# Kernel tuning notes

Measured on AMD Instinct MI355X. Metric: run time of the kernel, lower is better.

## Reference

```python
import jax, jax.numpy as jnp
import numpy as np

SCALE = 8.0  # sqrt(d_head=64)
NEG = -1e9


def setup_inputs() -> dict:
    key = jax.random.key(0)
    kq, kk, kv, km = jax.random.split(key, 4)
    B, H, S, D = 2, 16, 2048, 64
    q = jax.random.normal(kq, (B, H, S, D), dtype=jnp.float32)
    k = jax.random.normal(kk, (B, H, S, D), dtype=jnp.float32)
    v = jax.random.normal(kv, (B, H, S, D), dtype=jnp.float32)
    mask = jax.random.randint(km, (B, 1, 1, S), 0, 2, dtype=jnp.int32)
    return {"q": q, "k": k, "v": v, "mask": mask}


def reference(q, k, v, mask):
    # scores: [B,H,S,S]
    scores = jnp.einsum("bhqd,bhkd->bhqk", q / SCALE, k)
    scores = jnp.where(mask == 0, NEG, scores)
    attn = jax.nn.softmax(scores, axis=-1)  # dropout p=0 -> identity
    out = jnp.einsum("bhqk,bhkd->bhqd", attn, v)
    return (out, attn)
```

## Files before the change

### kernel.cpp

```cpp
#include <hip/hip_runtime.h>
#include <hip/hip_bf16.h>


#define S_LEN 2048
#define DH 64
#define QT 128
#define NCH (S_LEN / 64)

typedef __attribute__((ext_vector_type(8))) short  s16x8;
typedef __attribute__((ext_vector_type(8))) __bf16 bf16x8;
typedef __attribute__((ext_vector_type(4))) float  f32x4;
typedef __attribute__((ext_vector_type(2))) unsigned int u32x2;

__device__ __forceinline__ short f2bf(float x) {
    __hip_bfloat16 h = __float2bfloat16(x);
    return *reinterpret_cast<short*>(&h);
}
__device__ __forceinline__ unsigned pack2(float a, float b) {
    return (unsigned)(unsigned short)f2bf(a) | ((unsigned)(unsigned short)f2bf(b) << 16);
}
__device__ __forceinline__ bf16x8 ldfrag(const short* p) {
    s16x8 t = *(const s16x8*)p;
    return __builtin_bit_cast(bf16x8, t);
}
__device__ __forceinline__ int SW(int r, int c) { return r * 64 + (c ^ ((r & 7) << 3)); }

__global__ __launch_bounds__(512, 4) void sdpa_kernel(
    const float* __restrict__ q, const float* __restrict__ k,
    const float* __restrict__ v, const int* __restrict__ mask,
    float* __restrict__ out, float* __restrict__ attn)
{
    __shared__ __align__(16) short shQ[QT * 64];
    __shared__ __align__(16) short shK[2][64 * 64];
    __shared__ __align__(16) short shVt[2][64 * 64];
    __shared__ __align__(16) short shP[8][16 * 64];
    __shared__ __align__(16) float shMaskF[S_LEN];

    const int tid  = threadIdx.x;
    const int lane = tid & 63;
    const int w    = tid >> 6;
    const int l15  = lane & 15;
    const int lg   = lane >> 4;

    const int bh = blockIdx.y;
    const int b  = bh >> 4;
    const int q0 = blockIdx.x * QT;

    const float* qbase = q + ((size_t)bh * S_LEN + q0) * DH;
    const float* kbase = k + (size_t)bh * S_LEN * DH;
    const float* vbase = v + (size_t)bh * S_LEN * DH;
    float* attnbh = attn + (size_t)bh * S_LEN * S_LEN;

    for (int i = tid; i < S_LEN; i += 512)
        shMaskF[i] = (mask[b * S_LEN + i] != 0) ? 1.0f : 0.0f;
    {
        const int row = tid >> 2;
        const int d0  = (tid & 3) * 16;
        const float* src = qbase + row * DH + d0;
        const float4 a = *(const float4*)(src);
        const float4 bq = *(const float4*)(src + 4);
        const float4 c = *(const float4*)(src + 8);
        const float4 d = *(const float4*)(src + 12);
        s16x8 v0, v1;
        v0[0]=f2bf(a.x*0.125f);  v0[1]=f2bf(a.y*0.125f);  v0[2]=f2bf(a.z*0.125f);  v0[3]=f2bf(a.w*0.125f);
        v0[4]=f2bf(bq.x*0.125f); v0[5]=f2bf(bq.y*0.125f); v0[6]=f2bf(bq.z*0.125f); v0[7]=f2bf(bq.w*0.125f);
        v1[0]=f2bf(c.x*0.125f);  v1[1]=f2bf(c.y*0.125f);  v1[2]=f2bf(c.z*0.125f);  v1[3]=f2bf(c.w*0.125f);
        v1[4]=f2bf(d.x*0.125f);  v1[5]=f2bf(d.y*0.125f);  v1[6]=f2bf(d.z*0.125f);  v1[7]=f2bf(d.w*0.125f);
        *(s16x8*)&shQ[SW(row, d0)]     = v0;
        *(s16x8*)&shQ[SW(row, d0 + 8)] = v1;
    }

    const int krow = tid >> 3;
    const int kd0  = (tid & 7) * 8;
    auto loadK = [&](int c0, float4& a, float4& bb) {
        const float* src = kbase + (size_t)(c0 + krow) * DH + kd0;
        a  = *(const float4*)(src);
        bb = *(const float4*)(src + 4);
    };
    auto writeK = [&](short* dst, const float4& a, const float4& bb) {
        s16x8 vv;
        vv[0]=f2bf(a.x);  vv[1]=f2bf(a.y);  vv[2]=f2bf(a.z);  vv[3]=f2bf(a.w);
        vv[4]=f2bf(bb.x); vv[5]=f2bf(bb.y); vv[6]=f2bf(bb.z); vv[7]=f2bf(bb.w);
        *(s16x8*)&dst[SW(krow, kd0)] = vv;
    };
    const int vr0 = (tid & 31) * 2;
    const int vdg = tid >> 5;
    auto loadV = [&](int c0, float4& a, float4& bb) {
        const float* src = vbase + (size_t)(c0 + vr0) * DH + vdg * 4;
        a  = *(const float4*)(src);
        bb = *(const float4*)(src + DH);
    };
    auto writeVt = [&](short* dst, const float4& a, const float4& bb) {
        const float av[4] = {a.x, a.y, a.z, a.w};
        const float bv[4] = {bb.x, bb.y, bb.z, bb.w};
        int* dw = (int*)dst;
#pragma unroll
        for (int i = 0; i < 4; ++i) {
            const int d = vdg * 4 + i;
            dw[(d * 64 + (vr0 ^ ((d & 7) << 3))) >> 1] = (int)pack2(av[i], bv[i]);
        }
    };

    float4 ka, kb;
    loadK(0, ka, kb);
    writeK(shK[0], ka, kb);
    __syncthreads();

    const int qrow = w * 16 + l15;
    const bf16x8 qf0 = ldfrag(&shQ[SW(qrow, 8 * lg)]);
    const bf16x8 qf1 = ldfrag(&shQ[SW(qrow, 32 + 8 * lg)]);

    auto qkT = [&](const short* K, f32x4* s) {
#pragma unroll
        for (int ct = 0; ct < 4; ++ct) {
            const int kc = ct * 16 + l15;
            bf16x8 kf = ldfrag(&K[SW(kc, 8 * lg)]);
            s[ct] = __builtin_amdgcn_mfma_f32_16x16x32_bf16(kf, qf0, s[ct], 0, 0, 0);
            kf = ldfrag(&K[SW(kc, 32 + 8 * lg)]);
            s[ct] = __builtin_amdgcn_mfma_f32_16x16x32_bf16(kf, qf1, s[ct], 0, 0, 0);
        }
    };

    float lacc = 0.f;
    for (int t = 0; t < NCH; ++t) {
        const int cur = t & 1;
        if (t + 1 < NCH) loadK((t + 1) * 64, ka, kb);
        __syncthreads();
        f32x4 s[4] = {{0,0,0,0},{0,0,0,0},{0,0,0,0},{0,0,0,0}};
        qkT(shK[cur], s);
        const int c0 = t * 64;
#pragma unroll
        for (int ct = 0; ct < 4; ++ct) {
            const f32x4 mf = *(const f32x4*)&shMaskF[c0 + ct * 16 + lg * 4];
#pragma unroll
            for (int r = 0; r < 4; ++r)
                lacc = fmaf(__expf(s[ct][r]), mf[r], lacc);
        }
        if (t + 1 < NCH) writeK(shK[cur ^ 1], ka, kb);
    }
    lacc += __shfl_xor(lacc, 16);
    lacc += __shfl_xor(lacc, 32);
    const float lnInvl = -__logf(lacc);

    f32x4 oacc[4] = {{0,0,0,0},{0,0,0,0},{0,0,0,0},{0,0,0,0}};
    float4 va, vb;
    loadK(0, ka, kb);
    loadV(0, va, vb);
    writeK(shK[0], ka, kb);
    writeVt(shVt[0], va, vb);

    short* const shPw = shP[w];
    for (int t = 0; t < NCH; ++t) {
        const int cur = t & 1;
        if (t + 1 < NCH) { loadK((t + 1) * 64, ka, kb); loadV((t + 1) * 64, va, vb); }
        __syncthreads();
        f32x4 s[4] = {{0,0,0,0},{0,0,0,0},{0,0,0,0},{0,0,0,0}};
        qkT(shK[cur], s);

        const int c0 = t * 64;
        float* abase = attnbh + (size_t)(q0 + qrow) * S_LEN + c0;
#pragma unroll
        for (int ct = 0; ct < 4; ++ct) {
            const f32x4 mf = *(const f32x4*)&shMaskF[c0 + ct * 16 + lg * 4];
            f32x4 p;
#pragma unroll
            for (int r = 0; r < 4; ++r)
                p[r] = __expf(s[ct][r] + lnInvl) * mf[r];
            __builtin_nontemporal_store(p, (f32x4*)(abase + ct * 16 + lg * 4));
            u32x2 pk;
            pk[0] = pack2(p[0], p[1]);
            pk[1] = pack2(p[2], p[3]);
            *(u32x2*)&shPw[SW(l15, ct * 16 + lg * 4)] = pk;
        }
#pragma unroll
        for (int g = 0; g < 2; ++g) {
            const bf16x8 pf = ldfrag(&shPw[SW(l15, g * 32 + 8 * lg)]);
#pragma unroll
            for (int dt = 0; dt < 4; ++dt) {
                const bf16x8 af = ldfrag(&shVt[cur][SW(dt * 16 + l15, g * 32 + 8 * lg)]);
                oacc[dt] = __builtin_amdgcn_mfma_f32_16x16x32_bf16(af, pf, oacc[dt], 0, 0, 0);
            }
        }
        if (t + 1 < NCH) { writeK(shK[cur ^ 1], ka, kb); writeVt(shVt[cur ^ 1], va, vb); }
    }

    float* obase = out + ((size_t)bh * S_LEN + q0 + qrow) * DH;
#pragma unroll
    for (int dt = 0; dt < 4; ++dt)
        __builtin_nontemporal_store(oacc[dt], (f32x4*)(obase + dt * 16 + lg * 4));
}

extern "C" void kernel_launch(void* const* d_in, const int* in_sizes, int n_in,
                              void* d_out, int out_size, void* d_ws, size_t ws_size,
                              hipStream_t stream)
{
    const float* q    = (const float*)d_in[0];
    const float* k    = (const float*)d_in[1];
    const float* v    = (const float*)d_in[2];
    const int*   mask = (const int*)d_in[3];
    float* out  = (float*)d_out;
    float* attn = out + (size_t)2 * 16 * 2048 * 64;

    dim3 grid(S_LEN / QT, 2 * 16);
    sdpa_kernel<<<grid, dim3(512), 0, stream>>>(q, k, v, mask, out, attn);
}
```

Measured before the change: 197.2 us.

## Keep P in registers via 16x16x16 MFMA, drop Q/P shared buffers, remap grid

Q fragments are now loaded straight from global memory into registers instead of being staged through shared memory, and the per-wave P buffer is gone. The P tile from the QK^T accumulator is fed directly as the B operand of a 16x16x16 bf16 MFMA, since its register layout matches. This cuts LDS use and round-trips, and launch bounds are raised to allow 6 blocks per CU. The grid is flattened so consecutive blocks cover different heads. The trade-off is twice as many smaller MFMAs for PV, plus higher register pressure from the occupancy target.

```diff
diff --git a/kernel.cpp b/kernel.cpp
--- a/kernel.cpp
+++ b/kernel.cpp
@@ -8,6 +8,7 @@
 #define NCH (S_LEN / 64)
 
 typedef __attribute__((ext_vector_type(8))) short  s16x8;
+typedef __attribute__((ext_vector_type(4))) short  s16x4;
 typedef __attribute__((ext_vector_type(8))) __bf16 bf16x8;
 typedef __attribute__((ext_vector_type(4))) float  f32x4;
 typedef __attribute__((ext_vector_type(2))) unsigned int u32x2;
@@ -25,15 +26,13 @@
 }
 __device__ __forceinline__ int SW(int r, int c) { return r * 64 + (c ^ ((r & 7) << 3)); }
 
-__global__ __launch_bounds__(512, 4) void sdpa_kernel(
+__global__ __launch_bounds__(512, 6) void sdpa_kernel(
     const float* __restrict__ q, const float* __restrict__ k,
     const float* __restrict__ v, const int* __restrict__ mask,
     float* __restrict__ out, float* __restrict__ attn)
 {
-    __shared__ __align__(16) short shQ[QT * 64];
     __shared__ __align__(16) short shK[2][64 * 64];
     __shared__ __align__(16) short shVt[2][64 * 64];
-    __shared__ __align__(16) short shP[8][16 * 64];
     __shared__ __align__(16) float shMaskF[S_LEN];
 
     const int tid  = threadIdx.x;
@@ -42,9 +41,10 @@
     const int l15  = lane & 15;
     const int lg   = lane >> 4;
 
-    const int bh = blockIdx.y;
+    const int id = blockIdx.x;
+    const int bh = id & 31;
+    const int q0 = (id >> 5) * QT;
     const int b  = bh >> 4;
-    const int q0 = blockIdx.x * QT;
 
     const float* qbase = q + ((size_t)bh * S_LEN + q0) * DH;
     const float* kbase = k + (size_t)bh * S_LEN * DH;
@@ -53,21 +53,22 @@
 
     for (int i = tid; i < S_LEN; i += 512)
         shMaskF[i] = (mask[b * S_LEN + i] != 0) ? 1.0f : 0.0f;
+
+    const int qrow = w * 16 + l15;
+    bf16x8 qf0, qf1;
     {
-        const int row = tid >> 2;
-        const int d0  = (tid & 3) * 16;
-        const float* src = qbase + row * DH + d0;
-        const float4 a = *(const float4*)(src);
-        const float4 bq = *(const float4*)(src + 4);
-        const float4 c = *(const float4*)(src + 8);
-        const float4 d = *(const float4*)(src + 12);
-        s16x8 v0, v1;
-        v0[0]=f2bf(a.x*0.125f);  v0[1]=f2bf(a.y*0.125f);  v0[2]=f2bf(a.z*0.125f);  v0[3]=f2bf(a.w*0.125f);
-        v0[4]=f2bf(bq.x*0.125f); v0[5]=f2bf(bq.y*0.125f); v0[6]=f2bf(bq.z*0.125f); v0[7]=f2bf(bq.w*0.125f);
-        v1[0]=f2bf(c.x*0.125f);  v1[1]=f2bf(c.y*0.125f);  v1[2]=f2bf(c.z*0.125f);  v1[3]=f2bf(c.w*0.125f);
-        v1[4]=f2bf(d.x*0.125f);  v1[5]=f2bf(d.y*0.125f);  v1[6]=f2bf(d.z*0.125f);  v1[7]=f2bf(d.w*0.125f);
-        *(s16x8*)&shQ[SW(row, d0)]     = v0;
-        *(s16x8*)&shQ[SW(row, d0 + 8)] = v1;
+        const float* qp = qbase + qrow * DH + 8 * lg;
+        const float4 a0 = *(const float4*)(qp);
+        const float4 a1 = *(const float4*)(qp + 4);
+        const float4 b0 = *(const float4*)(qp + 32);
+        const float4 b1 = *(const float4*)(qp + 36);
+        s16x8 t0, t1;
+        t0[0]=f2bf(a0.x*0.125f); t0[1]=f2bf(a0.y*0.125f); t0[2]=f2bf(a0.z*0.125f); t0[3]=f2bf(a0.w*0.125f);
+        t0[4]=f2bf(a1.x*0.125f); t0[5]=f2bf(a1.y*0.125f); t0[6]=f2bf(a1.z*0.125f); t0[7]=f2bf(a1.w*0.125f);
+        t1[0]=f2bf(b0.x*0.125f); t1[1]=f2bf(b0.y*0.125f); t1[2]=f2bf(b0.z*0.125f); t1[3]=f2bf(b0.w*0.125f);
+        t1[4]=f2bf(b1.x*0.125f); t1[5]=f2bf(b1.y*0.125f); t1[6]=f2bf(b1.z*0.125f); t1[7]=f2bf(b1.w*0.125f);
+        qf0 = __builtin_bit_cast(bf16x8, t0);
+        qf1 = __builtin_bit_cast(bf16x8, t1);
     }
 
     const int krow = tid >> 3;
@@ -106,35 +107,25 @@
     writeK(shK[0], ka, kb);
     __syncthreads();
 
-    const int qrow = w * 16 + l15;
-    const bf16x8 qf0 = ldfrag(&shQ[SW(qrow, 8 * lg)]);
-    const bf16x8 qf1 = ldfrag(&shQ[SW(qrow, 32 + 8 * lg)]);
-
-    auto qkT = [&](const short* K, f32x4* s) {
-#pragma unroll
-        for (int ct = 0; ct < 4; ++ct) {
-            const int kc = ct * 16 + l15;
-            bf16x8 kf = ldfrag(&K[SW(kc, 8 * lg)]);
-            s[ct] = __builtin_amdgcn_mfma_f32_16x16x32_bf16(kf, qf0, s[ct], 0, 0, 0);
-            kf = ldfrag(&K[SW(kc, 32 + 8 * lg)]);
-            s[ct] = __builtin_amdgcn_mfma_f32_16x16x32_bf16(kf, qf1, s[ct], 0, 0, 0);
-        }
-    };
-
     float lacc = 0.f;
     for (int t = 0; t < NCH; ++t) {
         const int cur = t & 1;
         if (t + 1 < NCH) loadK((t + 1) * 64, ka, kb);
         __syncthreads();
-        f32x4 s[4] = {{0,0,0,0},{0,0,0,0},{0,0,0,0},{0,0,0,0}};
-        qkT(shK[cur], s);
+        const short* K = shK[cur];
         const int c0 = t * 64;
 #pragma unroll
         for (int ct = 0; ct < 4; ++ct) {
+            const int kc = ct * 16 + l15;
+            f32x4 s = {0.f, 0.f, 0.f, 0.f};
+            bf16x8 kf = ldfrag(&K[SW(kc, 8 * lg)]);
+            s = __builtin_amdgcn_mfma_f32_16x16x32_bf16(kf, qf0, s, 0, 0, 0);
+            kf = ldfrag(&K[SW(kc, 32 + 8 * lg)]);
+            s = __builtin_amdgcn_mfma_f32_16x16x32_bf16(kf, qf1, s, 0, 0, 0);
             const f32x4 mf = *(const f32x4*)&shMaskF[c0 + ct * 16 + lg * 4];
 #pragma unroll
             for (int r = 0; r < 4; ++r)
-                lacc = fmaf(__expf(s[ct][r]), mf[r], lacc);
+                lacc = fmaf(__expf(s[r]), mf[r], lacc);
         }
         if (t + 1 < NCH) writeK(shK[cur ^ 1], ka, kb);
     }
@@ -149,36 +140,39 @@
     writeK(shK[0], ka, kb);
     writeVt(shVt[0], va, vb);
 
-    short* const shPw = shP[w];
     for (int t = 0; t < NCH; ++t) {
         const int cur = t & 1;
         if (t + 1 < NCH) { loadK((t + 1) * 64, ka, kb); loadV((t + 1) * 64, va, vb); }
         __syncthreads();
-        f32x4 s[4] = {{0,0,0,0},{0,0,0,0},{0,0,0,0},{0,0,0,0}};
-        qkT(shK[cur], s);
-
+        const short* K  = shK[cur];
+        const short* Vt = shVt[cur];
         const int c0 = t * 64;
         float* abase = attnbh + (size_t)(q0 + qrow) * S_LEN + c0;
+
 #pragma unroll
         for (int ct = 0; ct < 4; ++ct) {
+            const int kc = ct * 16 + l15;
+            f32x4 s = {0.f, 0.f, 0.f, 0.f};
+            bf16x8 kf = ldfrag(&K[SW(kc, 8 * lg)]);
+            s = __builtin_amdgcn_mfma_f32_16x16x32_bf16(kf, qf0, s, 0, 0, 0);
+            kf = ldfrag(&K[SW(kc, 32 + 8 * lg)]);
+            s = __builtin_amdgcn_mfma_f32_16x16x32_bf16(kf, qf1, s, 0, 0, 0);
+
             const f32x4 mf = *(const f32x4*)&shMaskF[c0 + ct * 16 + lg * 4];
             f32x4 p;
 #pragma unroll
             for (int r = 0; r < 4; ++r)
-                p[r] = __expf(s[ct][r] + lnInvl) * mf[r];
+                p[r] = __expf(s[r] + lnInvl) * mf[r];
             __builtin_nontemporal_store(p, (f32x4*)(abase + ct * 16 + lg * 4));
+
             u32x2 pk;
             pk[0] = pack2(p[0], p[1]);
             pk[1] = pack2(p[2], p[3]);
-            *(u32x2*)&shPw[SW(l15, ct * 16 + lg * 4)] = pk;
-        }
-#pragma unroll
-        for (int g = 0; g < 2; ++g) {
-            const bf16x8 pf = ldfrag(&shPw[SW(l15, g * 32 + 8 * lg)]);
+            const s16x4 pf = __builtin_bit_cast(s16x4, pk);
 #pragma unroll
             for (int dt = 0; dt < 4; ++dt) {
-                const bf16x8 af = ldfrag(&shVt[cur][SW(dt * 16 + l15, g * 32 + 8 * lg)]);
-                oacc[dt] = __builtin_amdgcn_mfma_f32_16x16x32_bf16(af, pf, oacc[dt], 0, 0, 0);
+                const s16x4 af = *(const s16x4*)&Vt[SW(dt * 16 + l15, ct * 16 + 4 * lg)];
+                oacc[dt] = __builtin_amdgcn_mfma_f32_16x16x16bf16_1k(af, pf, oacc[dt], 0, 0, 0);
             }
         }
         if (t + 1 < NCH) { writeK(shK[cur ^ 1], ka, kb); writeVt(shVt[cur ^ 1], va, vb); }
@@ -201,6 +195,5 @@
     float* out  = (float*)d_out;
     float* attn = out + (size_t)2 * 16 * 2048 * 64;
 
-    dim3 grid(S_LEN / QT, 2 * 16);
-    sdpa_kernel<<<grid, dim3(512), 0, stream>>>(q, k, v, mask, out, attn);
+    sdpa_kernel<<<dim3((S_LEN / QT) * 32), dim3(512), 0, stream>>>(q, k, v, mask, out, attn);
 }
```

Result: slower. 272.9 us (+38.4%).
